# Optimization experiments

Measured on AMD Instinct MI355X. Metric: run time of the kernel, lower is better.

Reference implementation:

```python
import jax, jax.numpy as jnp
import numpy as np

B, D, N, S = 4096, 768, 8192, 4  # batch, embedding_dim, len(y)==cat rows, source_size


def setup_inputs() -> dict:
    key = jax.random.key(0)
    k1, k2, k3, k4 = jax.random.split(key, 4)
    batch_x = jax.random.normal(k1, (B, D), dtype=jnp.float32)
    cat = jax.random.normal(k2, (N, D), dtype=jnp.float32)
    y = jax.random.randint(k3, (N,), 0, 2, dtype=jnp.int32)
    # phi_srcs: xavier-uniform-like scale for (D, 1) params, stacked as [S, D]
    phi = jax.random.normal(k4, (S, D), dtype=jnp.float32) * 0.05
    bias = jnp.zeros((1,), dtype=jnp.float32)
    return {"batch_x": batch_x, "cat": cat, "y": y, "phi": phi, "bias": bias}


def reference(batch_x, cat, y, phi, bias):
    # con[n, b] = cat[n] . batch_x[b]   -> [N, B]
    con = jnp.einsum('nd,bd->nb', cat, batch_x)
    # F.normalize(con, p=4, dim=0): divide each column by its 4-norm (eps=1e-12)
    norm4 = jnp.power(jnp.sum(jnp.abs(con) ** 4, axis=0), 0.25)
    con = con / jnp.maximum(norm4, 1e-12)
    # softmax over all N rows (dim=0), per batch column
    con = jax.nn.softmax(con, axis=0)
    # chunk into S sources along the N axis: psi [S, N/S, B]
    psi = con.reshape(S, N // S, B)
    yf = y.astype(jnp.float32).reshape(S, N // S)  # y chunks [S, N/S]
    # theta_s = exp(x @ phi_s): [S, B]  (unnormalized, as in the original output path)
    theta = jnp.exp(jnp.einsum('bd,sd->sb', batch_x, phi))
    # per-source: sum_n y[s,n] * psi[s,n,b], then scale by theta[s,b]; sum over sources
    sum_matrix = jnp.sum(jnp.einsum('sn,snb->sb', yf, psi) * theta, axis=0)  # [B]
    y_hat = jax.nn.sigmoid(sum_matrix + bias)  # bias [1] broadcasts -> [B]
    return y_hat
```

## Files before the change

kernel.cpp:

```cpp
#include <hip/hip_runtime.h>
#include <hip/hip_bf16.h>
#include <stdint.h>

#define Bdim 4096
#define Ddim 768
#define Ndim 8192
#define Sdim 4

typedef __attribute__((ext_vector_type(4))) float floatx4;

__device__ inline unsigned short f2bf(float f) {
  unsigned u = __builtin_bit_cast(unsigned, f);
  unsigned r = (u + 0x7fffu + ((u >> 16) & 1u)) >> 16;
  return (unsigned short)r;
}
__device__ inline float bf2f(unsigned short s) {
  return __builtin_bit_cast(float, (unsigned)s << 16);
}

__device__ inline int pack_fp8x4(float4 v) {
  int r = __builtin_amdgcn_cvt_pk_fp8_f32(v.x, v.y, 0, 0);
  r = __builtin_amdgcn_cvt_pk_fp8_f32(v.z, v.w, r, 1);
  return r;
}

__device__ inline void async_copy16(const void* g, void* l) {
  __builtin_amdgcn_global_load_lds(
      (__attribute__((address_space(1))) void*)(g),
      (__attribute__((address_space(3))) void*)(l),
      16, 0, 0);
}

__global__ void convert_kernel(const float* __restrict__ x,
                               const float* __restrict__ cat,
                               const float* __restrict__ phi,
                               unsigned char* __restrict__ xq,
                               unsigned char* __restrict__ catq,
                               float* __restrict__ stats,
                               float* __restrict__ theta) {
  int gid = blockIdx.x * blockDim.x + threadIdx.x;
  int stride = gridDim.x * blockDim.x;
  const int nx4 = (Bdim * Ddim) / 4;
  const int nc4 = (Ndim * Ddim) / 4;
  for (int i = gid; i < nx4; i += stride)
    ((int*)xq)[i] = pack_fp8x4(((const float4*)x)[i]);
  for (int i = gid; i < nc4; i += stride)
    ((int*)catq)[i] = pack_fp8x4(((const float4*)cat)[i]);
  if (gid < 6 * Bdim) stats[gid] = 0.0f;

  int gw = gid >> 6;
  int lane = threadIdx.x & 63;
  if (gw < Bdim) {
    const float* xr = x + (size_t)gw * Ddim;
    float a0 = 0.f, a1 = 0.f, a2 = 0.f, a3 = 0.f;
    for (int d = lane; d < Ddim; d += 64) {
      float xv = xr[d];
      a0 = fmaf(xv, phi[d], a0);
      a1 = fmaf(xv, phi[Ddim + d], a1);
      a2 = fmaf(xv, phi[2 * Ddim + d], a2);
      a3 = fmaf(xv, phi[3 * Ddim + d], a3);
    }
#pragma unroll
    for (int off = 32; off > 0; off >>= 1) {
      a0 += __shfl_down(a0, off);
      a1 += __shfl_down(a1, off);
      a2 += __shfl_down(a2, off);
      a3 += __shfl_down(a3, off);
    }
    if (lane == 0) {
      theta[gw] = __expf(a0);
      theta[Bdim + gw] = __expf(a1);
      theta[2 * Bdim + gw] = __expf(a2);
      theta[3 * Bdim + gw] = __expf(a3);
    }
  }
}

__global__ __launch_bounds__(256) void gemm_bt_kernel(
    const unsigned char* __restrict__ A,
    const unsigned char* __restrict__ Bm,
    unsigned short* __restrict__ C,
    float* __restrict__ s4) {
  __shared__ unsigned char As[2][128 * 32];
  __shared__ unsigned char Bs[2][128 * 32];

  const int tid = threadIdx.x;
  const int wave = tid >> 6;
  const int lane = tid & 63;
  const int quad = lane >> 4;
  const int l16 = lane & 15;
  const int wm = (wave & 1) * 64;
  const int wn = (wave >> 1) * 64;
  const int m0 = blockIdx.x * 128;
  const int n0 = blockIdx.y * 128;

  floatx4 acc[4][4];
#pragma unroll
  for (int i = 0; i < 4; ++i)
#pragma unroll
    for (int j = 0; j < 4; ++j) acc[i][j] = (floatx4){0.f, 0.f, 0.f, 0.f};

  const int c = tid;
  const int r = c >> 1, colb = (c & 1) * 16;
  const unsigned char* a_src = A + (size_t)(m0 + r) * Ddim + colb;
  const unsigned char* b_src = Bm + (size_t)(n0 + r) * Ddim + colb;

  for (int k0 = 0; k0 < Ddim; k0 += 64) {
    async_copy16(a_src + k0, As[0] + c * 16);
    async_copy16(a_src + k0 + 32, As[1] + c * 16);
    async_copy16(b_src + k0, Bs[0] + c * 16);
    async_copy16(b_src + k0 + 32, Bs[1] + c * 16);
    __syncthreads();

#pragma unroll
    for (int h = 0; h < 2; ++h) {
      long af[4], bf[4];
#pragma unroll
      for (int mi = 0; mi < 4; ++mi)
        af[mi] = *(const long*)(As[h] + (wm + mi * 16 + l16) * 32 + quad * 8);
#pragma unroll
      for (int ni = 0; ni < 4; ++ni)
        bf[ni] = *(const long*)(Bs[h] + (wn + ni * 16 + l16) * 32 + quad * 8);
#pragma unroll
      for (int mi = 0; mi < 4; ++mi)
#pragma unroll
        for (int ni = 0; ni < 4; ++ni)
          acc[mi][ni] = __builtin_amdgcn_mfma_f32_16x16x32_fp8_fp8(
              af[mi], bf[ni], acc[mi][ni], 0, 0, 0);
    }
    __syncthreads();
  }

  float cs4[4] = {0.f, 0.f, 0.f, 0.f};
#pragma unroll
  for (int mi = 0; mi < 4; ++mi)
#pragma unroll
    for (int ni = 0; ni < 4; ++ni) {
      int row = m0 + wm + mi * 16 + quad * 4;
      int col = n0 + wn + ni * 16 + l16;
#pragma unroll
      for (int rr = 0; rr < 4; ++rr) {
        float cv = acc[mi][ni][rr];
        C[(size_t)(row + rr) * Bdim + col] = f2bf(cv);
        float c2 = cv * cv;
        cs4[ni] += c2 * c2;
      }
    }
#pragma unroll
  for (int ni = 0; ni < 4; ++ni) {
    float v = cs4[ni];
    v += __shfl_xor(v, 16);
    v += __shfl_xor(v, 32);
    if (quad == 0) atomicAdd(&s4[n0 + wn + ni * 16 + l16], v);
  }
}

__global__ void expsum_kernel(const unsigned short* __restrict__ con,
                              const float* __restrict__ s4,
                              const int* __restrict__ y,
                              float* __restrict__ denom,
                              float* __restrict__ numer) {
  int col0 = blockIdx.x * 1024 + threadIdx.x * 4;
  int n0 = blockIdx.y * 64;
  int src = n0 / (Ndim / Sdim);

  float4 s = *(const float4*)(s4 + col0);
  float inv0 = 1.0f / fmaxf(sqrtf(sqrtf(s.x)), 1e-12f);
  float inv1 = 1.0f / fmaxf(sqrtf(sqrtf(s.y)), 1e-12f);
  float inv2 = 1.0f / fmaxf(sqrtf(sqrtf(s.z)), 1e-12f);
  float inv3 = 1.0f / fmaxf(sqrtf(sqrtf(s.w)), 1e-12f);

  const unsigned short* p = con + (size_t)n0 * Bdim + col0;
  float d0 = 0.f, d1 = 0.f, d2 = 0.f, d3 = 0.f;
  float m0 = 0.f, m1 = 0.f, m2 = 0.f, m3 = 0.f;
#pragma unroll 8
  for (int i = 0; i < 64; ++i) {
    ushort4 v = *(const ushort4*)(p + (size_t)i * Bdim);
    float yv = (float)y[n0 + i];
    float e0 = __expf(bf2f(v.x) * inv0);
    float e1 = __expf(bf2f(v.y) * inv1);
    float e2 = __expf(bf2f(v.z) * inv2);
    float e3 = __expf(bf2f(v.w) * inv3);
    d0 += e0; d1 += e1; d2 += e2; d3 += e3;
    m0 += e0 * yv; m1 += e1 * yv; m2 += e2 * yv; m3 += e3 * yv;
  }
  atomicAdd(&denom[col0 + 0], d0);
  atomicAdd(&denom[col0 + 1], d1);
  atomicAdd(&denom[col0 + 2], d2);
  atomicAdd(&denom[col0 + 3], d3);
  float* np = numer + (size_t)src * Bdim + col0;
  atomicAdd(np + 0, m0);
  atomicAdd(np + 1, m1);
  atomicAdd(np + 2, m2);
  atomicAdd(np + 3, m3);
}

__global__ void finalize_kernel(const float* __restrict__ denom,
                                const float* __restrict__ numer,
                                const float* __restrict__ theta,
                                const float* __restrict__ bias,
                                float* __restrict__ out) {
  int b = blockIdx.x * 256 + threadIdx.x;
  float acc = 0.f;
#pragma unroll
  for (int si = 0; si < Sdim; ++si)
    acc += numer[si * Bdim + b] * theta[si * Bdim + b];
  float z = acc / denom[b] + bias[0];
  out[b] = 1.0f / (1.0f + __expf(-z));
}

extern "C" void kernel_launch(void* const* d_in, const int* in_sizes, int n_in,
                              void* d_out, int out_size, void* d_ws,
                              size_t ws_size, hipStream_t stream) {
  const float* batch_x = (const float*)d_in[0];
  const float* cat = (const float*)d_in[1];
  const int* y = (const int*)d_in[2];
  const float* phi = (const float*)d_in[3];
  const float* bias = (const float*)d_in[4];
  float* out = (float*)d_out;

  char* ws = (char*)d_ws;
  unsigned char* catq = (unsigned char*)ws;
  unsigned char* xq = catq + (size_t)Ndim * Ddim;
  unsigned short* con = (unsigned short*)(xq + (size_t)Bdim * Ddim);
  float* stats = (float*)(con + (size_t)Ndim * Bdim);
  float* s4 = stats;
  float* denom = s4 + Bdim;
  float* numer = denom + Bdim;
  float* theta = stats + 6 * Bdim;

  convert_kernel<<<2048, 256, 0, stream>>>(batch_x, cat, phi, xq, catq, stats,
                                           theta);

  dim3 g2(Ndim / 128, Bdim / 128);
  gemm_bt_kernel<<<g2, 256, 0, stream>>>(catq, xq, con, s4);

  dim3 g3(Bdim / 1024, Ndim / 64);
  expsum_kernel<<<g3, 256, 0, stream>>>(con, s4, y, denom, numer);

  finalize_kernel<<<Bdim / 256, 256, 0, stream>>>(denom, numer, theta, bias,
                                                  out);
}
```

Baseline: 181.1 us.

## Use MI355 scaled 16x16x128 FP8 MFMA with K=128 tiles and swizzled LDS

Replaces the 16x16x32 FP8 MFMA with the gfx950 scaled 16x16x128 f8f6f4 MFMA using unit scales. The K step per iteration grows from 64 to 128 and the LDS tiles become 128x128 bytes. Global-to-LDS copies use a row-interleaved layout so each lane reads its 32 K-bytes with two 16-byte LDS loads. The goal is fewer MFMA issues and fewer loop iterations and barriers per tile. In exchange it uses more shared memory per block, and the fragment layout must match what the new instruction expects.

```diff
diff --git a/kernel.cpp b/kernel.cpp
--- a/kernel.cpp
+++ b/kernel.cpp
@@ -8,6 +8,8 @@
 #define Sdim 4
 
 typedef __attribute__((ext_vector_type(4))) float floatx4;
+typedef __attribute__((ext_vector_type(8))) int int8v;
+typedef __attribute__((ext_vector_type(4))) int int4v;
 
 __device__ inline unsigned short f2bf(float f) {
   unsigned u = __builtin_bit_cast(unsigned, f);
@@ -81,8 +83,8 @@
     const unsigned char* __restrict__ Bm,
     unsigned short* __restrict__ C,
     float* __restrict__ s4) {
-  __shared__ unsigned char As[2][128 * 32];
-  __shared__ unsigned char Bs[2][128 * 32];
+  __shared__ unsigned char As[128 * 128];
+  __shared__ unsigned char Bs[128 * 128];
 
   const int tid = threadIdx.x;
   const int wave = tid >> 6;
@@ -100,34 +102,50 @@
 #pragma unroll
     for (int j = 0; j < 4; ++j) acc[i][j] = (floatx4){0.f, 0.f, 0.f, 0.f};
 
-  const int c = tid;
-  const int r = c >> 1, colb = (c & 1) * 16;
-  const unsigned char* a_src = A + (size_t)(m0 + r) * Ddim + colb;
-  const unsigned char* b_src = Bm + (size_t)(n0 + r) * Ddim + colb;
-
-  for (int k0 = 0; k0 < Ddim; k0 += 64) {
-    async_copy16(a_src + k0, As[0] + c * 16);
-    async_copy16(a_src + k0 + 32, As[1] + c * 16);
-    async_copy16(b_src + k0, Bs[0] + c * 16);
-    async_copy16(b_src + k0 + 32, Bs[1] + c * 16);
+  const unsigned char* a_src[4];
+  const unsigned char* b_src[4];
+#pragma unroll
+  for (int i = 0; i < 4; ++i) {
+    int p = tid + 256 * i;
+    int row = ((p >> 6) << 3) + (p & 7);
+    int colb = ((p >> 3) & 7) * 16;
+    a_src[i] = A + (size_t)(m0 + row) * Ddim + colb;
+    b_src[i] = Bm + (size_t)(n0 + row) * Ddim + colb;
+  }
+
+  for (int k0 = 0; k0 < Ddim; k0 += 128) {
+#pragma unroll
+    for (int i = 0; i < 4; ++i) {
+      async_copy16(a_src[i] + k0, As + (tid + 256 * i) * 16);
+      async_copy16(b_src[i] + k0, Bs + (tid + 256 * i) * 16);
+    }
     __syncthreads();
 
-#pragma unroll
-    for (int h = 0; h < 2; ++h) {
-      long af[4], bf[4];
-#pragma unroll
-      for (int mi = 0; mi < 4; ++mi)
-        af[mi] = *(const long*)(As[h] + (wm + mi * 16 + l16) * 32 + quad * 8);
+    int8v af[4], bf[4];
+#pragma unroll
+    for (int mi = 0; mi < 4; ++mi) {
+      int r = wm + mi * 16 + l16;
+      int base = ((r >> 3) << 10) + quad * 256 + (r & 7) * 16;
+      int4v lo = *(const int4v*)(As + base);
+      int4v hi = *(const int4v*)(As + base + 128);
+      af[mi] = __builtin_shufflevector(lo, hi, 0, 1, 2, 3, 4, 5, 6, 7);
+    }
+#pragma unroll
+    for (int ni = 0; ni < 4; ++ni) {
+      int r = wn + ni * 16 + l16;
+      int base = ((r >> 3) << 10) + quad * 256 + (r & 7) * 16;
+      int4v lo = *(const int4v*)(Bs + base);
+      int4v hi = *(const int4v*)(Bs + base + 128);
+      bf[ni] = __builtin_shufflevector(lo, hi, 0, 1, 2, 3, 4, 5, 6, 7);
+    }
+#pragma unroll
+    for (int mi = 0; mi < 4; ++mi)
 #pragma unroll
       for (int ni = 0; ni < 4; ++ni)
-        bf[ni] = *(const long*)(Bs[h] + (wn + ni * 16 + l16) * 32 + quad * 8);
-#pragma unroll
-      for (int mi = 0; mi < 4; ++mi)
-#pragma unroll
-        for (int ni = 0; ni < 4; ++ni)
-          acc[mi][ni] = __builtin_amdgcn_mfma_f32_16x16x32_fp8_fp8(
-              af[mi], bf[ni], acc[mi][ni], 0, 0, 0);
-    }
+        acc[mi][ni] = __builtin_amdgcn_mfma_scale_f32_16x16x128_f8f6f4(
+            af[mi], bf[ni], acc[mi][ni], 0, 0,
+            0, 0x7f7f7f7f,
+            0, 0x7f7f7f7f);
     __syncthreads();
   }
 
```

Result: faster. 177.1 us (-2.2%).
